# Optimization experiments

Measured on AMD Instinct MI355X. Metric: run time of the kernel, lower is better.

## Reference

```python
import jax, jax.numpy as jnp
import numpy as np

B, N, D = 256, 50, 128
N_NODE, MAX_ATTR = 50000, 2000
ALPHA = 0.2  # LeakyReLU negative slope
STDV = 1.0 / np.sqrt(D)  # reset_parameters uniform(-stdv, stdv)
NEG = -9e15


def setup_inputs() -> dict:
    key = jax.random.key(0)
    ks = jax.random.split(key, 10)
    uni = lambda k, shp: jax.random.uniform(k, shp, jnp.float32, -STDV, STDV)
    return {
        "inputs": jax.random.randint(ks[0], (B, N), 0, N_NODE),
        "adj": jax.random.randint(ks[1], (B, N, N), 0, 5),
        "mask_item": jax.random.randint(ks[2], (B, N), 0, 2),
        "A_attr_sess": jax.random.normal(ks[3], (B, MAX_ATTR), jnp.float32),
        "embedding": uni(ks[4], (N_NODE, D)),
        "attr_embedding": uni(ks[5], (MAX_ATTR, D)),
        "a0": uni(ks[6], (D,)),
        "a1": uni(ks[7], (D,)),
        "a2": uni(ks[8], (D,)),
        "a3": uni(ks[9], (D,)),
    }


def reference(inputs, adj, mask_item, A_attr_sess, embedding, attr_embedding, a0, a1, a2, a3):
    h = embedding[inputs]  # [B, N, D]
    # (h.repeat(1,1,N) * h.repeat(1,N,1)).view(B,N,N,D) == outer elementwise product h_i * h_j
    a_in = jax.nn.leaky_relu(h[:, :, None, :] * h[:, None, :, :], ALPHA)  # [B,N,N,D]
    a_all = jnp.stack([a0, a1, a2, a3], axis=-1)  # [D, 4]
    e = jnp.einsum('bijd,dk->bijk', a_in, a_all)  # [B,N,N,4]
    alpha = jnp.full(adj.shape, NEG, dtype=e.dtype)
    alpha = jnp.where(adj == 1, e[..., 0], alpha)
    alpha = jnp.where(adj == 2, e[..., 1], alpha)
    alpha = jnp.where(adj == 3, e[..., 2], alpha)
    alpha = jnp.where(adj == 4, e[..., 3], alpha)
    alpha = jax.nn.softmax(alpha, axis=-1)
    output = jnp.einsum('bij,bjd->bid', alpha, h)  # [B, N, D]
    attr_sess = A_attr_sess @ attr_embedding  # [B, D]
    return output, attr_sess
```

## Files before the change

### kernel.cpp

```cpp
#include <hip/hip_runtime.h>
#include <math.h>

#define BB 256
#define NN 50
#define DD 128
#define MAXA 2000
#define NEGV -9e15f
#define NATTR 256

#define H_S   136
#define HT_S  72
#define AL_S  72

#define H_OFF   0
#define HT_OFF  (64 * H_S)
#define AL_OFF  (HT_OFF + 128 * HT_S)
#define ADJ_OFF (AL_OFF + 64 * AL_S)
#define LDS_US  (ADJ_OFF + 64 * 64)

typedef __attribute__((ext_vector_type(8))) short        s8b;
typedef __attribute__((ext_vector_type(4))) float        f32x4;
typedef __attribute__((ext_vector_type(4))) unsigned int u32x4;

static __device__ __forceinline__ unsigned int pack2(float lo, float hi) {
    unsigned int r;
    asm("v_cvt_pk_bf16_f32 %0, %1, %2" : "=v"(r) : "v"(lo), "v"(hi));
    return r;
}
static __device__ __forceinline__ float bf2f(unsigned int s) {
    return __uint_as_float(s << 16);
}
static __device__ __forceinline__ f32x4 mfma16(u32x4 a, u32x4 b, f32x4 c) {
    return __builtin_amdgcn_mfma_f32_16x16x32_bf16(
        __builtin_bit_cast(s8b, a), __builtin_bit_cast(s8b, b), c, 0, 0, 0);
}

__global__ __launch_bounds__(256) void sg_fused_kernel(
    const int* __restrict__ inputs,
    const int* __restrict__ adj,
    const float* __restrict__ A_attr,
    const float* __restrict__ embedding,
    const float* __restrict__ attr_emb,
    const float* __restrict__ a0,
    const float* __restrict__ a1,
    const float* __restrict__ a2,
    const float* __restrict__ a3,
    float* __restrict__ out,
    float* __restrict__ ws)
{
    __shared__ __align__(16) unsigned short sh[LDS_US];
    const int blk  = blockIdx.x;
    const int tid  = threadIdx.x;
    const int w    = tid >> 6;
    const int lane = tid & 63;
    const int g    = lane >> 4;
    const int c    = lane & 15;
    const int goff = g * 8;

    if (blk < BB) {
        const int b = blk;

        const int  i_   = lane;
        const bool live = (i_ < NN);
        int node = 0;
        if (live) node = inputs[b * NN + i_];
        float4 gv[8];
        #pragma unroll
        for (int n = 0; n < 8; ++n) {
            gv[n] = make_float4(0.f, 0.f, 0.f, 0.f);
            if (live) gv[n] = *(const float4*)(embedding + (size_t)node * DD + (w * 8 + n) * 4);
        }
        for (int idx = tid; idx < 4096; idx += 256) {
            const int i = idx >> 6, j = idx & 63;
            int a = 0;
            if (i < NN && j < NN) a = adj[(size_t)b * (NN * NN) + i * NN + j];
            sh[ADJ_OFF + idx] = (unsigned short)a;
        }
        #pragma unroll
        for (int n = 0; n < 8; ++n) {
            const int d4 = w * 8 + n;
            const unsigned int pk01 = pack2(gv[n].x, gv[n].y);
            const unsigned int pk23 = pack2(gv[n].z, gv[n].w);
            *(uint2*)(sh + H_OFF + i_ * H_S + d4 * 4) = make_uint2(pk01, pk23);
            sh[HT_OFF + (d4 * 4 + 0) * HT_S + i_] = (unsigned short)pk01;
            sh[HT_OFF + (d4 * 4 + 1) * HT_S + i_] = (unsigned short)(pk01 >> 16);
            sh[HT_OFF + (d4 * 4 + 2) * HT_S + i_] = (unsigned short)pk23;
            sh[HT_OFF + (d4 * 4 + 3) * HT_S + i_] = (unsigned short)(pk23 >> 16);
        }
        __syncthreads();

        u32x4 hA[4];
        float hf[4][8], hb[4][8];
        #pragma unroll
        for (int dt = 0; dt < 4; ++dt) {
            hA[dt] = *(const u32x4*)(const void*)(sh + H_OFF + (w * 16 + c) * H_S + dt * 32 + goff);
            #pragma unroll
            for (int p = 0; p < 4; ++p) {
                const unsigned int hp = hA[dt][p];
                hf[dt][2 * p]     = bf2f(hp & 0xffffu);
                hf[dt][2 * p + 1] = bf2f(hp >> 16);
                hb[dt][2 * p]     = fabsf(hf[dt][2 * p]);
                hb[dt][2 * p + 1] = fabsf(hf[dt][2 * p + 1]);
            }
        }
        f32x4 accS[4][4];
        #pragma unroll
        for (int jt = 0; jt < 4; ++jt)
            #pragma unroll
            for (int k = 0; k < 4; ++k) accS[jt][k] = (f32x4){0.f, 0.f, 0.f, 0.f};

        #pragma unroll
        for (int pass = 0; pass < 2; ++pass) {
            u32x4 Uf[4][2], Vf[4][2];
            #pragma unroll
            for (int kk = 0; kk < 2; ++kk) {
                const int k = pass * 2 + kk;
                const float* ap = (k == 0) ? a0 : (k == 1) ? a1 : (k == 2) ? a2 : a3;
                #pragma unroll
                for (int dt = 0; dt < 4; ++dt) {
                    const float4 aL = *(const float4*)(ap + dt * 32 + goff);
                    const float4 aH = *(const float4*)(ap + dt * 32 + goff + 4);
                    const float a8[8] = {aL.x, aL.y, aL.z, aL.w, aH.x, aH.y, aH.z, aH.w};
                    u32x4 U, V;
                    #pragma unroll
                    for (int p = 0; p < 4; ++p) {
                        U[p] = pack2(0.6f * a8[2 * p] * hf[dt][2 * p],
                                     0.6f * a8[2 * p + 1] * hf[dt][2 * p + 1]);
                        V[p] = pack2(0.4f * a8[2 * p] * hb[dt][2 * p],
                                     0.4f * a8[2 * p + 1] * hb[dt][2 * p + 1]);
                    }
                    Uf[dt][kk] = U; Vf[dt][kk] = V;
                }
            }
            #pragma unroll
            for (int jt = 0; jt < 4; ++jt) {
                #pragma unroll
                for (int dt = 0; dt < 4; ++dt) {
                    const u32x4 hB = *(const u32x4*)(const void*)(sh + H_OFF + (jt * 16 + c) * H_S + dt * 32 + goff);
                    u32x4 hBa;
                    #pragma unroll
                    for (int p = 0; p < 4; ++p) hBa[p] = hB[p] & 0x7fff7fffu;
                    accS[jt][pass * 2 + 0] = mfma16(Uf[dt][0], hB,  accS[jt][pass * 2 + 0]);
                    accS[jt][pass * 2 + 0] = mfma16(Vf[dt][0], hBa, accS[jt][pass * 2 + 0]);
                    accS[jt][pass * 2 + 1] = mfma16(Uf[dt][1], hB,  accS[jt][pass * 2 + 1]);
                    accS[jt][pass * 2 + 1] = mfma16(Vf[dt][1], hBa, accS[jt][pass * 2 + 1]);
                }
            }
        }

        float s_[4][4];
        #pragma unroll
        for (int jt = 0; jt < 4; ++jt) {
            #pragma unroll
            for (int reg = 0; reg < 4; ++reg) {
                const int il = w * 16 + g * 4 + reg;
                const int j  = jt * 16 + c;
                const int a  = (int)sh[ADJ_OFF + il * 64 + j];
                float sv = (a == 1) ? accS[jt][0][reg] : (a == 2) ? accS[jt][1][reg]
                         : (a == 3) ? accS[jt][2][reg] : (a == 4) ? accS[jt][3][reg] : NEGV;
                if (j >= NN) sv = -INFINITY;
                s_[jt][reg] = sv;
            }
        }
        #pragma unroll
        for (int reg = 0; reg < 4; ++reg) {
            float m = fmaxf(fmaxf(s_[0][reg], s_[1][reg]), fmaxf(s_[2][reg], s_[3][reg]));
            m = fmaxf(m, __shfl_xor(m, 1));
            m = fmaxf(m, __shfl_xor(m, 2));
            m = fmaxf(m, __shfl_xor(m, 4));
            m = fmaxf(m, __shfl_xor(m, 8));
            const float p0 = __expf(s_[0][reg] - m);
            const float p1 = __expf(s_[1][reg] - m);
            const float p2 = __expf(s_[2][reg] - m);
            const float p3 = __expf(s_[3][reg] - m);
            float sum = (p0 + p1) + (p2 + p3);
            sum += __shfl_xor(sum, 1);
            sum += __shfl_xor(sum, 2);
            sum += __shfl_xor(sum, 4);
            sum += __shfl_xor(sum, 8);
            const float r  = 1.0f / sum;
            const int  il  = w * 16 + g * 4 + reg;
            sh[AL_OFF + il * AL_S +  0 + c] = (unsigned short)pack2(p0 * r, p0 * r);
            sh[AL_OFF + il * AL_S + 16 + c] = (unsigned short)pack2(p1 * r, p1 * r);
            sh[AL_OFF + il * AL_S + 32 + c] = (unsigned short)pack2(p2 * r, p2 * r);
            sh[AL_OFF + il * AL_S + 48 + c] = (unsigned short)pack2(p3 * r, p3 * r);
        }

        const int il = w * 16 + c;
        const u32x4 pa0 = *(const u32x4*)(const void*)(sh + AL_OFF + il * AL_S + goff);
        const u32x4 pa1 = *(const u32x4*)(const void*)(sh + AL_OFF + il * AL_S + 32 + goff);
        #pragma unroll
        for (int nt = 0; nt < 8; ++nt) {
            const u32x4 v0 = *(const u32x4*)(const void*)(sh + HT_OFF + (nt * 16 + c) * HT_S + goff);
            const u32x4 v1 = *(const u32x4*)(const void*)(sh + HT_OFF + (nt * 16 + c) * HT_S + 32 + goff);
            f32x4 accp = (f32x4){0.f, 0.f, 0.f, 0.f};
            accp = mfma16(pa0, v0, accp);
            accp = mfma16(pa1, v1, accp);
            #pragma unroll
            for (int reg = 0; reg < 4; ++reg) {
                const int ig = w * 16 + g * 4 + reg;
                if (ig < NN)
                    out[((size_t)b * NN + ig) * DD + nt * 16 + c] = accp[reg];
            }
        }
    } else {
        const int ablk = blk - BB;
        const int mg = ablk >> 4;
        const int ks = ablk & 15;
        const int m0 = mg * 16;
        const int wd = w * 32;
        const float* Arow = A_attr + (size_t)(m0 + c) * MAXA;

        f32x4 acc2[2];
        acc2[0] = (f32x4){0.f, 0.f, 0.f, 0.f};
        acc2[1] = (f32x4){0.f, 0.f, 0.f, 0.f};

        auto do_chunk = [&](int k0, bool guard) {
            float4 aL = make_float4(0.f, 0.f, 0.f, 0.f);
            float4 aH = make_float4(0.f, 0.f, 0.f, 0.f);
            if (!guard || k0 + goff + 3 < MAXA) aL = *(const float4*)(Arow + k0 + goff);
            if (!guard || k0 + goff + 7 < MAXA) aH = *(const float4*)(Arow + k0 + goff + 4);
            u32x4 af;
            af[0] = pack2(aL.x, aL.y); af[1] = pack2(aL.z, aL.w);
            af[2] = pack2(aH.x, aH.y); af[3] = pack2(aH.z, aH.w);
            #pragma unroll
            for (int ntl = 0; ntl < 2; ++ntl) {
                const int col = wd + ntl * 16 + c;
                float ev[8];
                #pragma unroll
                for (int p = 0; p < 8; ++p) {
                    const int kr = k0 + goff + p;
                    ev[p] = (!guard || kr < MAXA) ? attr_emb[(size_t)kr * DD + col] : 0.f;
                }
                u32x4 bf_;
                bf_[0] = pack2(ev[0], ev[1]); bf_[1] = pack2(ev[2], ev[3]);
                bf_[2] = pack2(ev[4], ev[5]); bf_[3] = pack2(ev[6], ev[7]);
                acc2[ntl] = mfma16(af, bf_, acc2[ntl]);
            }
        };
        #pragma unroll
        for (int q = 0; q < 3; ++q) do_chunk((ks + q * 16) * 32, false);
        if (ks + 48 < 63) do_chunk((ks + 48) * 32, (ks + 48) == 62);

        float* pt = ws + (size_t)ablk * (16 * DD);
        #pragma unroll
        for (int ntl = 0; ntl < 2; ++ntl)
            #pragma unroll
            for (int reg = 0; reg < 4; ++reg)
                pt[(g * 4 + reg) * DD + wd + ntl * 16 + c] = acc2[ntl][reg];
    }
}

__global__ __launch_bounds__(256) void attr_reduce_kernel(
    const float* __restrict__ ws, float* __restrict__ attr_out)
{
    const int idx = blockIdx.x * 256 + threadIdx.x;
    const int m  = idx >> 7;
    const int d  = idx & 127;
    const int mg = m >> 4;
    const int r  = m & 15;
    const size_t base = (size_t)mg * 16 * (16 * DD) + r * DD + d;
    float v = 0.f;
    #pragma unroll
    for (int ks = 0; ks < 16; ++ks)
        v += ws[base + (size_t)ks * (16 * DD)];
    attr_out[(size_t)m * DD + d] = v;
}

extern "C" void kernel_launch(void* const* d_in, const int* in_sizes, int n_in,
                              void* d_out, int out_size, void* d_ws, size_t ws_size,
                              hipStream_t stream) {
    const int*   inputs    = (const int*)  d_in[0];
    const int*   adj       = (const int*)  d_in[1];
    const float* A_attr    = (const float*)d_in[3];
    const float* embedding = (const float*)d_in[4];
    const float* attr_emb  = (const float*)d_in[5];
    const float* a0        = (const float*)d_in[6];
    const float* a1        = (const float*)d_in[7];
    const float* a2        = (const float*)d_in[8];
    const float* a3        = (const float*)d_in[9];

    float* out      = (float*)d_out;
    float* attr_out = out + (size_t)BB * NN * DD;
    float* ws       = (float*)d_ws;

    sg_fused_kernel<<<BB + NATTR, 256, 0, stream>>>(inputs, adj, A_attr, embedding,
                                                    attr_emb, a0, a1, a2, a3,
                                                    out, ws);
    attr_reduce_kernel<<<128, 256, 0, stream>>>(ws, attr_out);
}
```

Baseline: 21.73 us.

## Split attr partial GEMM into own kernel and fuse reduction into GAT kernel

Moves the attribute partial-product GEMM into a separate first kernel and fuses the partial-sum reduction into the GAT kernel as extra leading blocks. The reduction itself is vectorised to float4. The GAT score loop is restructured to iterate over the d-tiles once, computing all four U/V operands per tile instead of two passes with precomputed hf/hb arrays. This is meant to cut register pressure and the separate reduce launch. The cost is that the GAT work no longer shares a launch with the attribute GEMM and must wait behind it.

New measurement: 22.73 us. 4.6% more time.

```diff
diff --git a/kernel.cpp b/kernel.cpp
--- a/kernel.cpp
+++ b/kernel.cpp
@@ -7,6 +7,7 @@
 #define MAXA 2000
 #define NEGV -9e15f
 #define NATTR 256
+#define NRED 32
 
 #define H_S   136
 #define HT_S  72
@@ -35,21 +36,12 @@
         __builtin_bit_cast(s8b, a), __builtin_bit_cast(s8b, b), c, 0, 0, 0);
 }
 
-__global__ __launch_bounds__(256) void sg_fused_kernel(
-    const int* __restrict__ inputs,
-    const int* __restrict__ adj,
+__global__ __launch_bounds__(256) void attr_part_kernel(
     const float* __restrict__ A_attr,
-    const float* __restrict__ embedding,
     const float* __restrict__ attr_emb,
-    const float* __restrict__ a0,
-    const float* __restrict__ a1,
-    const float* __restrict__ a2,
-    const float* __restrict__ a3,
-    float* __restrict__ out,
     float* __restrict__ ws)
 {
-    __shared__ __align__(16) unsigned short sh[LDS_US];
-    const int blk  = blockIdx.x;
+    const int ablk = blockIdx.x;
     const int tid  = threadIdx.x;
     const int w    = tid >> 6;
     const int lane = tid & 63;
@@ -57,214 +49,226 @@
     const int c    = lane & 15;
     const int goff = g * 8;
 
-    if (blk < BB) {
-        const int b = blk;
-
-        const int  i_   = lane;
-        const bool live = (i_ < NN);
-        int node = 0;
-        if (live) node = inputs[b * NN + i_];
-        float4 gv[8];
-        #pragma unroll
-        for (int n = 0; n < 8; ++n) {
-            gv[n] = make_float4(0.f, 0.f, 0.f, 0.f);
-            if (live) gv[n] = *(const float4*)(embedding + (size_t)node * DD + (w * 8 + n) * 4);
-        }
-        for (int idx = tid; idx < 4096; idx += 256) {
-            const int i = idx >> 6, j = idx & 63;
-            int a = 0;
-            if (i < NN && j < NN) a = adj[(size_t)b * (NN * NN) + i * NN + j];
-            sh[ADJ_OFF + idx] = (unsigned short)a;
-        }
-        #pragma unroll
-        for (int n = 0; n < 8; ++n) {
-            const int d4 = w * 8 + n;
-            const unsigned int pk01 = pack2(gv[n].x, gv[n].y);
-            const unsigned int pk23 = pack2(gv[n].z, gv[n].w);
-            *(uint2*)(sh + H_OFF + i_ * H_S + d4 * 4) = make_uint2(pk01, pk23);
-            sh[HT_OFF + (d4 * 4 + 0) * HT_S + i_] = (unsigned short)pk01;
-            sh[HT_OFF + (d4 * 4 + 1) * HT_S + i_] = (unsigned short)(pk01 >> 16);
-            sh[HT_OFF + (d4 * 4 + 2) * HT_S + i_] = (unsigned short)pk23;
-            sh[HT_OFF + (d4 * 4 + 3) * HT_S + i_] = (unsigned short)(pk23 >> 16);
-        }
-        __syncthreads();
-
-        u32x4 hA[4];
-        float hf[4][8], hb[4][8];
-        #pragma unroll
-        for (int dt = 0; dt < 4; ++dt) {
-            hA[dt] = *(const u32x4*)(const void*)(sh + H_OFF + (w * 16 + c) * H_S + dt * 32 + goff);
+    const int mg = ablk >> 4;
+    const int ks = ablk & 15;
+    const int m0 = mg * 16;
+    const int wd = w * 32;
+    const float* Arow = A_attr + (size_t)(m0 + c) * MAXA;
+
+    f32x4 acc2[2];
+    acc2[0] = (f32x4){0.f, 0.f, 0.f, 0.f};
+    acc2[1] = (f32x4){0.f, 0.f, 0.f, 0.f};
+
+    auto do_chunk = [&](int k0, bool guard) {
+        float4 aL = make_float4(0.f, 0.f, 0.f, 0.f);
+        float4 aH = make_float4(0.f, 0.f, 0.f, 0.f);
+        if (!guard || k0 + goff + 3 < MAXA) aL = *(const float4*)(Arow + k0 + goff);
+        if (!guard || k0 + goff + 7 < MAXA) aH = *(const float4*)(Arow + k0 + goff + 4);
+        u32x4 af;
+        af[0] = pack2(aL.x, aL.y); af[1] = pack2(aL.z, aL.w);
+        af[2] = pack2(aH.x, aH.y); af[3] = pack2(aH.z, aH.w);
+        #pragma unroll
+        for (int ntl = 0; ntl < 2; ++ntl) {
+            const int col = wd + ntl * 16 + c;
+            float ev[8];
+            #pragma unroll
+            for (int p = 0; p < 8; ++p) {
+                const int kr = k0 + goff + p;
+                ev[p] = (!guard || kr < MAXA) ? attr_emb[(size_t)kr * DD + col] : 0.f;
+            }
+            u32x4 bf_;
+            bf_[0] = pack2(ev[0], ev[1]); bf_[1] = pack2(ev[2], ev[3]);
+            bf_[2] = pack2(ev[4], ev[5]); bf_[3] = pack2(ev[6], ev[7]);
+            acc2[ntl] = mfma16(af, bf_, acc2[ntl]);
+        }
+    };
+    #pragma unroll
+    for (int q = 0; q < 3; ++q) do_chunk((ks + q * 16) * 32, false);
+    if (ks + 48 < 63) do_chunk((ks + 48) * 32, (ks + 48) == 62);
+
+    float* pt = ws + (size_t)ablk * (16 * DD);
+    #pragma unroll
+    for (int ntl = 0; ntl < 2; ++ntl)
+        #pragma unroll
+        for (int reg = 0; reg < 4; ++reg)
+            pt[(g * 4 + reg) * DD + wd + ntl * 16 + c] = acc2[ntl][reg];
+}
+
+__global__ __launch_bounds__(256) void sg_gat_kernel(
+    const int* __restrict__ inputs,
+    const int* __restrict__ adj,
+    const float* __restrict__ embedding,
+    const float* __restrict__ a0,
+    const float* __restrict__ a1,
+    const float* __restrict__ a2,
+    const float* __restrict__ a3,
+    const float* __restrict__ ws,
+    float* __restrict__ out,
+    float* __restrict__ attr_out)
+{
+    __shared__ __align__(16) unsigned short sh[LDS_US];
+    const int blk  = blockIdx.x;
+    const int tid  = threadIdx.x;
+
+    if (blk < NRED) {
+        const int idx = blk * 256 + tid;
+        const int m  = idx >> 5;
+        const int d4 = idx & 31;
+        const int mg = m >> 4;
+        const int r  = m & 15;
+        const float4* base = (const float4*)ws + (size_t)(mg * 16) * 512 + r * 32 + d4;
+        float4 v = make_float4(0.f, 0.f, 0.f, 0.f);
+        #pragma unroll
+        for (int ks = 0; ks < 16; ++ks) {
+            const float4 t = base[(size_t)ks * 512];
+            v.x += t.x; v.y += t.y; v.z += t.z; v.w += t.w;
+        }
+        ((float4*)attr_out)[(size_t)m * 32 + d4] = v;
+        return;
+    }
+
+    const int b    = blk - NRED;
+    const int w    = tid >> 6;
+    const int lane = tid & 63;
+    const int g    = lane >> 4;
+    const int c    = lane & 15;
+    const int goff = g * 8;
+
+    const int  i_   = lane;
+    const bool live = (i_ < NN);
+    int node = 0;
+    if (live) node = inputs[b * NN + i_];
+    float4 gv[8];
+    #pragma unroll
+    for (int n = 0; n < 8; ++n) {
+        gv[n] = make_float4(0.f, 0.f, 0.f, 0.f);
+        if (live) gv[n] = *(const float4*)(embedding + (size_t)node * DD + (w * 8 + n) * 4);
+    }
+    for (int idx = tid; idx < 4096; idx += 256) {
+        const int i = idx >> 6, j = idx & 63;
+        int a = 0;
+        if (i < NN && j < NN) a = adj[(size_t)b * (NN * NN) + i * NN + j];
+        sh[ADJ_OFF + idx] = (unsigned short)a;
+    }
+    #pragma unroll
+    for (int n = 0; n < 8; ++n) {
+        const int d4 = w * 8 + n;
+        const unsigned int pk01 = pack2(gv[n].x, gv[n].y);
+        const unsigned int pk23 = pack2(gv[n].z, gv[n].w);
+        *(uint2*)(sh + H_OFF + i_ * H_S + d4 * 4) = make_uint2(pk01, pk23);
+        sh[HT_OFF + (d4 * 4 + 0) * HT_S + i_] = (unsigned short)pk01;
+        sh[HT_OFF + (d4 * 4 + 1) * HT_S + i_] = (unsigned short)(pk01 >> 16);
+        sh[HT_OFF + (d4 * 4 + 2) * HT_S + i_] = (unsigned short)pk23;
+        sh[HT_OFF + (d4 * 4 + 3) * HT_S + i_] = (unsigned short)(pk23 >> 16);
+    }
+    __syncthreads();
+
+    u32x4 hA[4];
+    #pragma unroll
+    for (int dt = 0; dt < 4; ++dt)
+        hA[dt] = *(const u32x4*)(const void*)(sh + H_OFF + (w * 16 + c) * H_S + dt * 32 + goff);
+
+    f32x4 accS[4][4];
+    #pragma unroll
+    for (int jt = 0; jt < 4; ++jt)
+        #pragma unroll
+        for (int k = 0; k < 4; ++k) accS[jt][k] = (f32x4){0.f, 0.f, 0.f, 0.f};
+
+    #pragma unroll
+    for (int dt = 0; dt < 4; ++dt) {
+        float hf8[8], hb8[8];
+        #pragma unroll
+        for (int p = 0; p < 4; ++p) {
+            const unsigned int hp = hA[dt][p];
+            hf8[2 * p]     = bf2f(hp & 0xffffu);
+            hf8[2 * p + 1] = bf2f(hp >> 16);
+            hb8[2 * p]     = fabsf(hf8[2 * p]);
+            hb8[2 * p + 1] = fabsf(hf8[2 * p + 1]);
+        }
+        u32x4 U[4], V[4];
+        #pragma unroll
+        for (int k = 0; k < 4; ++k) {
+            const float* ap = (k == 0) ? a0 : (k == 1) ? a1 : (k == 2) ? a2 : a3;
+            const float4 aL = *(const float4*)(ap + dt * 32 + goff);
+            const float4 aH = *(const float4*)(ap + dt * 32 + goff + 4);
+            const float a8[8] = {aL.x, aL.y, aL.z, aL.w, aH.x, aH.y, aH.z, aH.w};
             #pragma unroll
             for (int p = 0; p < 4; ++p) {
-                const unsigned int hp = hA[dt][p];
-                hf[dt][2 * p]     = bf2f(hp & 0xffffu);
-                hf[dt][2 * p + 1] = bf2f(hp >> 16);
-                hb[dt][2 * p]     = fabsf(hf[dt][2 * p]);
-                hb[dt][2 * p + 1] = fabsf(hf[dt][2 * p + 1]);
+                U[k][p] = pack2(0.6f * a8[2 * p] * hf8[2 * p],
+                                0.6f * a8[2 * p + 1] * hf8[2 * p + 1]);
+                V[k][p] = pack2(0.4f * a8[2 * p] * hb8[2 * p],
+                                0.4f * a8[2 * p + 1] * hb8[2 * p + 1]);
             }
         }
-        f32x4 accS[4][4];
-        #pragma unroll
-        for (int jt = 0; jt < 4; ++jt)
-            #pragma unroll
-            for (int k = 0; k < 4; ++k) accS[jt][k] = (f32x4){0.f, 0.f, 0.f, 0.f};
-
-        #pragma unroll
-        for (int pass = 0; pass < 2; ++pass) {
-            u32x4 Uf[4][2], Vf[4][2];
-            #pragma unroll
-            for (int kk = 0; kk < 2; ++kk) {
-                const int k = pass * 2 + kk;
-                const float* ap = (k == 0) ? a0 : (k == 1) ? a1 : (k == 2) ? a2 : a3;
-                #pragma unroll
-                for (int dt = 0; dt < 4; ++dt) {
-                    const float4 aL = *(const float4*)(ap + dt * 32 + goff);
-                    const float4 aH = *(const float4*)(ap + dt * 32 + goff + 4);
-                    const float a8[8] = {aL.x, aL.y, aL.z, aL.w, aH.x, aH.y, aH.z, aH.w};
-                    u32x4 U, V;
-                    #pragma unroll
-                    for (int p = 0; p < 4; ++p) {
-                        U[p] = pack2(0.6f * a8[2 * p] * hf[dt][2 * p],
-                                     0.6f * a8[2 * p + 1] * hf[dt][2 * p + 1]);
-                        V[p] = pack2(0.4f * a8[2 * p] * hb[dt][2 * p],
-                                     0.4f * a8[2 * p + 1] * hb[dt][2 * p + 1]);
-                    }
-                    Uf[dt][kk] = U; Vf[dt][kk] = V;
-                }
+        #pragma unroll
+        for (int jt = 0; jt < 4; ++jt) {
+            const u32x4 hB = *(const u32x4*)(const void*)(sh + H_OFF + (jt * 16 + c) * H_S + dt * 32 + goff);
+            u32x4 hBa;
+            #pragma unroll
+            for (int p = 0; p < 4; ++p) hBa[p] = hB[p] & 0x7fff7fffu;
+            #pragma unroll
+            for (int k = 0; k < 4; ++k) {
+                accS[jt][k] = mfma16(U[k], hB,  accS[jt][k]);
+                accS[jt][k] = mfma16(V[k], hBa, accS[jt][k]);
             }
-            #pragma unroll
-            for (int jt = 0; jt < 4; ++jt) {
-                #pragma unroll
-                for (int dt = 0; dt < 4; ++dt) {
-                    const u32x4 hB = *(const u32x4*)(const void*)(sh + H_OFF + (jt * 16 + c) * H_S + dt * 32 + goff);
-                    u32x4 hBa;
-                    #pragma unroll
-                    for (int p = 0; p < 4; ++p) hBa[p] = hB[p] & 0x7fff7fffu;
-                    accS[jt][pass * 2 + 0] = mfma16(Uf[dt][0], hB,  accS[jt][pass * 2 + 0]);
-                    accS[jt][pass * 2 + 0] = mfma16(Vf[dt][0], hBa, accS[jt][pass * 2 + 0]);
-                    accS[jt][pass * 2 + 1] = mfma16(Uf[dt][1], hB,  accS[jt][pass * 2 + 1]);
-                    accS[jt][pass * 2 + 1] = mfma16(Vf[dt][1], hBa, accS[jt][pass * 2 + 1]);
-                }
-            }
-        }
-
-        float s_[4][4];
-        #pragma unroll
-        for (int jt = 0; jt < 4; ++jt) {
-            #pragma unroll
-            for (int reg = 0; reg < 4; ++reg) {
-                const int il = w * 16 + g * 4 + reg;
-                const int j  = jt * 16 + c;
-                const int a  = (int)sh[ADJ_OFF + il * 64 + j];
-                float sv = (a == 1) ? accS[jt][0][reg] : (a == 2) ? accS[jt][1][reg]
-                         : (a == 3) ? accS[jt][2][reg] : (a == 4) ? accS[jt][3][reg] : NEGV;
-                if (j >= NN) sv = -INFINITY;
-                s_[jt][reg] = sv;
-            }
-        }
+        }
+    }
+
+    float s_[4][4];
+    #pragma unroll
+    for (int jt = 0; jt < 4; ++jt) {
         #pragma unroll
         for (int reg = 0; reg < 4; ++reg) {
-            float m = fmaxf(fmaxf(s_[0][reg], s_[1][reg]), fmaxf(s_[2][reg], s_[3][reg]));
-            m = fmaxf(m, __shfl_xor(m, 1));
-            m = fmaxf(m, __shfl_xor(m, 2));
-            m = fmaxf(m, __shfl_xor(m, 4));
-            m = fmaxf(m, __shfl_xor(m, 8));
-            const float p0 = __expf(s_[0][reg] - m);
-            const float p1 = __expf(s_[1][reg] - m);
-            const float p2 = __expf(s_[2][reg] - m);
-            const float p3 = __expf(s_[3][reg] - m);
-            float sum = (p0 + p1) + (p2 + p3);
-            sum += __shfl_xor(sum, 1);
-            sum += __shfl_xor(sum, 2);
-            sum += __shfl_xor(sum, 4);
-            sum += __shfl_xor(sum, 8);
-            const float r  = 1.0f / sum;
-            const int  il  = w * 16 + g * 4 + reg;
-            sh[AL_OFF + il * AL_S +  0 + c] = (unsigned short)pack2(p0 * r, p0 * r);
-            sh[AL_OFF + il * AL_S + 16 + c] = (unsigned short)pack2(p1 * r, p1 * r);
-            sh[AL_OFF + il * AL_S + 32 + c] = (unsigned short)pack2(p2 * r, p2 * r);
-            sh[AL_OFF + il * AL_S + 48 + c] = (unsigned short)pack2(p3 * r, p3 * r);
-        }
-
-        const int il = w * 16 + c;
-        const u32x4 pa0 = *(const u32x4*)(const void*)(sh + AL_OFF + il * AL_S + goff);
-        const u32x4 pa1 = *(const u32x4*)(const void*)(sh + AL_OFF + il * AL_S + 32 + goff);
-        #pragma unroll
-        for (int nt = 0; nt < 8; ++nt) {
-            const u32x4 v0 = *(const u32x4*)(const void*)(sh + HT_OFF + (nt * 16 + c) * HT_S + goff);
-            const u32x4 v1 = *(const u32x4*)(const void*)(sh + HT_OFF + (nt * 16 + c) * HT_S + 32 + goff);
-            f32x4 accp = (f32x4){0.f, 0.f, 0.f, 0.f};
-            accp = mfma16(pa0, v0, accp);
-            accp = mfma16(pa1, v1, accp);
-            #pragma unroll
-            for (int reg = 0; reg < 4; ++reg) {
-                const int ig = w * 16 + g * 4 + reg;
-                if (ig < NN)
-                    out[((size_t)b * NN + ig) * DD + nt * 16 + c] = accp[reg];
-            }
-        }
-    } else {
-        const int ablk = blk - BB;
-        const int mg = ablk >> 4;
-        const int ks = ablk & 15;
-        const int m0 = mg * 16;
-        const int wd = w * 32;
-        const float* Arow = A_attr + (size_t)(m0 + c) * MAXA;
-
-        f32x4 acc2[2];
-        acc2[0] = (f32x4){0.f, 0.f, 0.f, 0.f};
-        acc2[1] = (f32x4){0.f, 0.f, 0.f, 0.f};
-
-        auto do_chunk = [&](int k0, bool guard) {
-            float4 aL = make_float4(0.f, 0.f, 0.f, 0.f);
-            float4 aH = make_float4(0.f, 0.f, 0.f, 0.f);
-            if (!guard || k0 + goff + 3 < MAXA) aL = *(const float4*)(Arow + k0 + goff);
-            if (!guard || k0 + goff + 7 < MAXA) aH = *(const float4*)(Arow + k0 + goff + 4);
-            u32x4 af;
-            af[0] = pack2(aL.x, aL.y); af[1] = pack2(aL.z, aL.w);
-            af[2] = pack2(aH.x, aH.y); af[3] = pack2(aH.z, aH.w);
-            #pragma unroll
-            for (int ntl = 0; ntl < 2; ++ntl) {
-                const int col = wd + ntl * 16 + c;
-                float ev[8];
-                #pragma unroll
-                for (int p = 0; p < 8; ++p) {
-                    const int kr = k0 + goff + p;
-                    ev[p] = (!guard || kr < MAXA) ? attr_emb[(size_t)kr * DD + col] : 0.f;
-                }
-                u32x4 bf_;
-                bf_[0] = pack2(ev[0], ev[1]); bf_[1] = pack2(ev[2], ev[3]);
-                bf_[2] = pack2(ev[4], ev[5]); bf_[3] = pack2(ev[6], ev[7]);
-                acc2[ntl] = mfma16(af, bf_, acc2[ntl]);
-            }
-        };
-        #pragma unroll
-        for (int q = 0; q < 3; ++q) do_chunk((ks + q * 16) * 32, false);
-        if (ks + 48 < 63) do_chunk((ks + 48) * 32, (ks + 48) == 62);
-
-        float* pt = ws + (size_t)ablk * (16 * DD);
-        #pragma unroll
-        for (int ntl = 0; ntl < 2; ++ntl)
-            #pragma unroll
-            for (int reg = 0; reg < 4; ++reg)
-                pt[(g * 4 + reg) * DD + wd + ntl * 16 + c] = acc2[ntl][reg];
-    }
-}
-
-__global__ __launch_bounds__(256) void attr_reduce_kernel(
-    const float* __restrict__ ws, float* __restrict__ attr_out)
-{
-    const int idx = blockIdx.x * 256 + threadIdx.x;
-    const int m  = idx >> 7;
-    const int d  = idx & 127;
-    const int mg = m >> 4;
-    const int r  = m & 15;
-    const size_t base = (size_t)mg * 16 * (16 * DD) + r * DD + d;
-    float v = 0.f;
-    #pragma unroll
-    for (int ks = 0; ks < 16; ++ks)
-        v += ws[base + (size_t)ks * (16 * DD)];
-    attr_out[(size_t)m * DD + d] = v;
+            const int il = w * 16 + g * 4 + reg;
+            const int j  = jt * 16 + c;
+            const int a  = (int)sh[ADJ_OFF + il * 64 + j];
+            float sv = (a == 1) ? accS[jt][0][reg] : (a == 2) ? accS[jt][1][reg]
+                     : (a == 3) ? accS[jt][2][reg] : (a == 4) ? accS[jt][3][reg] : NEGV;
+            if (j >= NN) sv = -INFINITY;
+            s_[jt][reg] = sv;
+        }
+    }
+    #pragma unroll
+    for (int reg = 0; reg < 4; ++reg) {
+        float m = fmaxf(fmaxf(s_[0][reg], s_[1][reg]), fmaxf(s_[2][reg], s_[3][reg]));
+        m = fmaxf(m, __shfl_xor(m, 1));
+        m = fmaxf(m, __shfl_xor(m, 2));
+        m = fmaxf(m, __shfl_xor(m, 4));
+        m = fmaxf(m, __shfl_xor(m, 8));
+        const float p0 = __expf(s_[0][reg] - m);
+        const float p1 = __expf(s_[1][reg] - m);
+        const float p2 = __expf(s_[2][reg] - m);
+        const float p3 = __expf(s_[3][reg] - m);
+        float sum = (p0 + p1) + (p2 + p3);
+        sum += __shfl_xor(sum, 1);
+        sum += __shfl_xor(sum, 2);
+        sum += __shfl_xor(sum, 4);
+        sum += __shfl_xor(sum, 8);
+        const float r  = 1.0f / sum;
+        const int  il  = w * 16 + g * 4 + reg;
+        sh[AL_OFF + il * AL_S +  0 + c] = (unsigned short)pack2(p0 * r, p0 * r);
+        sh[AL_OFF + il * AL_S + 16 + c] = (unsigned short)pack2(p1 * r, p1 * r);
+        sh[AL_OFF + il * AL_S + 32 + c] = (unsigned short)pack2(p2 * r, p2 * r);
+        sh[AL_OFF + il * AL_S + 48 + c] = (unsigned short)pack2(p3 * r, p3 * r);
+    }
+
+    const int il = w * 16 + c;
+    const u32x4 pa0 = *(const u32x4*)(const void*)(sh + AL_OFF + il * AL_S + goff);
+    const u32x4 pa1 = *(const u32x4*)(const void*)(sh + AL_OFF + il * AL_S + 32 + goff);
+    #pragma unroll
+    for (int nt = 0; nt < 8; ++nt) {
+        const u32x4 v0 = *(const u32x4*)(const void*)(sh + HT_OFF + (nt * 16 + c) * HT_S + goff);
+        const u32x4 v1 = *(const u32x4*)(const void*)(sh + HT_OFF + (nt * 16 + c) * HT_S + 32 + goff);
+        f32x4 accp = (f32x4){0.f, 0.f, 0.f, 0.f};
+        accp = mfma16(pa0, v0, accp);
+        accp = mfma16(pa1, v1, accp);
+        #pragma unroll
+        for (int reg = 0; reg < 4; ++reg) {
+            const int ig = w * 16 + g * 4 + reg;
+            if (ig < NN)
+                out[((size_t)b * NN + ig) * DD + nt * 16 + c] = accp[reg];
+        }
+    }
 }
 
 extern "C" void kernel_launch(void* const* d_in, const int* in_sizes, int n_in,
@@ -284,8 +288,8 @@
     float* attr_out = out + (size_t)BB * NN * DD;
     float* ws       = (float*)d_ws;
 
-    sg_fused_kernel<<<BB + NATTR, 256, 0, stream>>>(inputs, adj, A_attr, embedding,
-                                                    attr_emb, a0, a1, a2, a3,
-                                                    out, ws);
-    attr_reduce_kernel<<<128, 256, 0, stream>>>(ws, attr_out);
-}
+    attr_part_kernel<<<NATTR, 256, 0, stream>>>(A_attr, attr_emb, ws);
+    sg_gat_kernel<<<NRED + BB, 256, 0, stream>>>(inputs, adj, embedding,
+                                                 a0, a1, a2, a3, ws,
+                                                 out, attr_out);
+}
```
